# Kernel optimization log

Measured on AMD Instinct MI355X. Metric: run time of the kernel, lower is better.

Reference implementation:

```python
import jax, jax.numpy as jnp
import numpy as np

B, T, E = 4, 2048, 2048
NH, NKV, HD = 16, 4, 128
THETA = 10000.0


def _rope(x, pos_ids, theta):
    # x: [b, h, t, hd]; pos_ids: [b, t]; theta: [hd/2]
    ang = pos_ids[:, None, :, None].astype(jnp.float32) * theta  # [b,1,t,hd/2]
    cos, sin = jnp.cos(ang), jnp.sin(ang)
    x1, x2 = x[..., ::2], x[..., 1::2]
    # interleave rotated pairs back to [..., hd]
    rot = jnp.stack([x1 * cos - x2 * sin, x1 * sin + x2 * cos], axis=-1)
    return rot.reshape(x.shape)


def setup_inputs() -> dict:
    key = jax.random.key(0)
    ks = jax.random.split(key, 10)
    s = 0.02
    x = jax.random.normal(ks[0], (B, T, E), dtype=jnp.float32)
    attention_mask = jax.random.randint(ks[1], (B, T, T), 0, 2, dtype=jnp.int32)
    # torch nn.Linear weights stored here as [in, out] (y = x @ W + b)
    Wq = jax.random.normal(ks[2], (E, E), dtype=jnp.float32) * s
    bq = jnp.zeros((E,), dtype=jnp.float32)
    Wk = jax.random.normal(ks[3], (E, NKV * HD), dtype=jnp.float32) * s
    bk = jnp.zeros((NKV * HD,), dtype=jnp.float32)
    Wv = jax.random.normal(ks[4], (E, NKV * HD), dtype=jnp.float32) * s
    bv = jnp.zeros((NKV * HD,), dtype=jnp.float32)
    Wo = jax.random.normal(ks[5], (E, E), dtype=jnp.float32) * s
    bo = jnp.zeros((E,), dtype=jnp.float32)
    return {"x": x, "attention_mask": attention_mask, "Wq": Wq, "bq": bq,
            "Wk": Wk, "bk": bk, "Wv": Wv, "bv": bv, "Wo": Wo, "bo": bo}


def reference(x, attention_mask, Wq, bq, Wk, bk, Wv, bv, Wo, bo):
    b, t = x.shape[0], x.shape[1]
    # faithful to original: plain reshape (view), NOT transpose-based head split
    q = (x @ Wq + bq).reshape(b, NH, t, HD)
    k = (x @ Wk + bk).reshape(b, NKV, t, HD)
    v = (x @ Wv + bv).reshape(b, NKV, t, HD)
    theta = THETA ** (-jnp.arange(0, HD, 2, dtype=jnp.float32) / HD)
    pos = jnp.broadcast_to(jnp.arange(t), (b, t))
    # original RoPE.forward is wrapped in @torch.no_grad() -> stop_gradient
    k = jax.lax.stop_gradient(_rope(k, pos, theta))
    v = jax.lax.stop_gradient(_rope(v, pos, theta))  # note: RoPE applied to V too
    g = NH // NKV
    k = jnp.tile(k, (1, g, 1, 1))  # torch .repeat tiles kv heads
    v = jnp.tile(v, (1, g, 1, 1))
    # original divides by head_dim ** (-0.5) == multiply by sqrt(head_dim)
    scores = jnp.einsum('bhqd,bhkd->bhqk', q, k) * (HD ** 0.5)
    scores = jnp.where(attention_mask[:, None, :, :] == 0, jnp.float32(1e-9), scores)
    attn = jax.nn.softmax(scores, axis=-1)  # dropout inactive (eval mode)
    out = jnp.einsum('bhqk,bhkd->bhqd', attn, v)
    out = out.transpose(0, 2, 1, 3).reshape(b, t, NH * HD)
    return out @ Wo + bo
```

## Files before the change

kernel.cpp:

```cpp
#include <hip/hip_runtime.h>
#include <math.h>

constexpr int Bc   = 4;
constexpr int Tc   = 2048;
constexpr int Ec   = 2048;
constexpr int NHc  = 16;
constexpr int NKVc = 4;
constexpr int HDc  = 128;
constexpr int KVEc = NKVc * HDc;

typedef __attribute__((ext_vector_type(8))) short bf16x8;
typedef __attribute__((ext_vector_type(4))) short short4v;
typedef __attribute__((ext_vector_type(4))) float f32x4;

__device__ __forceinline__ short f2bf(float f) {
    union { float f; unsigned u; } v; v.f = f;
    unsigned r = v.u + 0x7FFF + ((v.u >> 16) & 1);
    return (short)(r >> 16);
}
__device__ __forceinline__ float bf2f(short s) {
    union { unsigned u; float f; } v; v.u = ((unsigned)(unsigned short)s) << 16;
    return v.f;
}
__device__ __forceinline__ float ex2(float x) {
    float r; asm("v_exp_f32 %0, %1" : "=v"(r) : "v"(x)); return r;
}
__device__ __forceinline__ void gload16(const void* g, void* l) {
    __builtin_amdgcn_global_load_lds(
        (const __attribute__((address_space(1))) unsigned*)g,
        (__attribute__((address_space(3))) unsigned*)l, 16, 0, 0);
}

__global__ __launch_bounds__(256)
void convert_split(const float* __restrict__ X, short* __restrict__ Xhi,
                   short* __restrict__ Xlo)
{
    int i = blockIdx.x * 256 + threadIdx.x;
    float4 v = ((const float4*)X)[i];
    float fv[4] = {v.x, v.y, v.z, v.w};
    short4v hi, lo;
    #pragma unroll
    for (int j = 0; j < 4; ++j) {
        hi[j] = f2bf(fv[j]);
        lo[j] = f2bf(fv[j] - bf2f(hi[j]));
    }
    ((short4v*)Xhi)[i] = hi;
    ((short4v*)Xlo)[i] = lo;
}

__global__ __launch_bounds__(256)
void transpose_split(const float* __restrict__ W, short* __restrict__ WThi,
                     short* __restrict__ WTlo, int K, int N)
{
    __shared__ float Ls[32][33];
    const int k0 = blockIdx.x * 32, n0 = blockIdx.y * 32;
    const int t = threadIdx.x;
    const int r = t >> 3, c4 = (t & 7) << 2;
    float4 v = *(const float4*)(W + (size_t)(k0 + r) * N + n0 + c4);
    Ls[r][c4 + 0] = v.x; Ls[r][c4 + 1] = v.y;
    Ls[r][c4 + 2] = v.z; Ls[r][c4 + 3] = v.w;
    __syncthreads();
    short4v hi, lo;
    #pragma unroll
    for (int i = 0; i < 4; ++i) {
        float f = Ls[c4 + i][r];
        hi[i] = f2bf(f);
        lo[i] = f2bf(f - bf2f(hi[i]));
    }
    *(short4v*)(WThi + (size_t)(n0 + r) * K + k0 + c4) = hi;
    if (WTlo) *(short4v*)(WTlo + (size_t)(n0 + r) * K + k0 + c4) = lo;
}

__global__ __launch_bounds__(256)
void mask_bits(const int* __restrict__ mask, unsigned long long* __restrict__ Mb)
{
    const int widx = blockIdx.x * 4 + (threadIdx.x >> 6);
    const int L = threadIdx.x & 63;
    const int m = mask[(size_t)widx * 64 + L];
    unsigned long long bits = __ballot(m != 0);
    if (L == 0) Mb[widx] = bits;
}

template <bool SPLIT, bool QOUT>
__global__ __launch_bounds__(256, 2)
void gemm_mfma(const short* __restrict__ Ahi, const short* __restrict__ Alo,
               const short* __restrict__ Bhi, const short* __restrict__ Blo,
               const float* __restrict__ bias, float* __restrict__ C,
               short* __restrict__ Chi, short* __restrict__ Clo,
               int M, int N, int K)
{
    __shared__ short AsH[128 * 32];
    __shared__ short BsH[128 * 32];
    __shared__ short AsL[SPLIT ? 128 * 32 : 8];
    __shared__ short BsL[SPLIT ? 128 * 32 : 8];

    const int t = threadIdx.x;
    const int w = t >> 6, L = t & 63;
    const int l16 = L & 15, quad = L >> 4;
    const int wr = w >> 1, wc = w & 1;
    const int bm = blockIdx.x * 128, bn = blockIdx.y * 128;

    const int sm = L >> 2;
    const int sq = ((L & 3) - (sm >> 2)) & 3;
    const int scol = sq * 8;

    f32x4 acc[4][4];
    #pragma unroll
    for (int mi = 0; mi < 4; ++mi)
        #pragma unroll
        for (int ni = 0; ni < 4; ++ni) acc[mi][ni] = (f32x4){0, 0, 0, 0};

    const int fxor = (quad + (l16 >> 2)) & 3;

    for (int k0 = 0; k0 < K; k0 += 32) {
        __syncthreads();
        #pragma unroll
        for (int i = 0; i < 2; ++i) {
            const int wl = w * 2 + i;
            const size_t ra = (size_t)(bm + wl * 16 + sm) * K + k0 + scol;
            const size_t rb = (size_t)(bn + wl * 16 + sm) * K + k0 + scol;
            gload16(Ahi + ra, &AsH[wl * 512]);
            gload16(Bhi + rb, &BsH[wl * 512]);
            if (SPLIT) {
                gload16(Alo + ra, &AsL[wl * 512]);
                gload16(Blo + rb, &BsL[wl * 512]);
            }
        }
        __syncthreads();

        bf16x8 ah[4], bh[4], al[4], bl[4];
        #pragma unroll
        for (int mi = 0; mi < 4; ++mi) {
            const int ch = ((wr * 4 + mi) * 64 + l16 * 4 + fxor) * 8;
            ah[mi] = *(const bf16x8*)&AsH[ch];
            if (SPLIT) al[mi] = *(const bf16x8*)&AsL[ch];
        }
        #pragma unroll
        for (int ni = 0; ni < 4; ++ni) {
            const int ch = ((wc * 4 + ni) * 64 + l16 * 4 + fxor) * 8;
            bh[ni] = *(const bf16x8*)&BsH[ch];
            if (SPLIT) bl[ni] = *(const bf16x8*)&BsL[ch];
        }
        #pragma unroll
        for (int mi = 0; mi < 4; ++mi)
            #pragma unroll
            for (int ni = 0; ni < 4; ++ni) {
                acc[mi][ni] = __builtin_amdgcn_mfma_f32_16x16x32_bf16(
                    ah[mi], bh[ni], acc[mi][ni], 0, 0, 0);
                if (SPLIT) {
                    acc[mi][ni] = __builtin_amdgcn_mfma_f32_16x16x32_bf16(
                        al[mi], bh[ni], acc[mi][ni], 0, 0, 0);
                    acc[mi][ni] = __builtin_amdgcn_mfma_f32_16x16x32_bf16(
                        ah[mi], bl[ni], acc[mi][ni], 0, 0, 0);
                }
            }
    }

    #pragma unroll
    for (int ni = 0; ni < 4; ++ni) {
        const int col = bn + wc * 64 + ni * 16 + l16;
        const float bv = bias[col];
        #pragma unroll
        for (int mi = 0; mi < 4; ++mi) {
            #pragma unroll
            for (int r = 0; r < 4; ++r) {
                const int row = bm + wr * 64 + mi * 16 + quad * 4 + r;
                const float f = acc[mi][ni][r] + bv;
                if (QOUT) {
                    const short hi = f2bf(f);
                    Chi[(size_t)row * N + col] = hi;
                    Clo[(size_t)row * N + col] = f2bf(f - bf2f(hi));
                } else {
                    C[(size_t)row * N + col] = f;
                }
            }
        }
    }
}

__global__ __launch_bounds__(256)
void rope_k(const float* __restrict__ X2d, short* __restrict__ Khi,
            short* __restrict__ Klo)
{
    const int idx = blockIdx.x * 256 + threadIdx.x;
    const int j  = idx & 63;
    const int tk = (idx >> 6) & (Tc - 1);
    const int kh = (idx >> 17) & (NKVc - 1);
    const int bb = idx >> 19;
    const int row = (kh << 9) + (tk >> 2);
    const int col = ((tk & 3) << 7) + (j << 1);
    const float* src = X2d + ((size_t)bb * Tc + row) * KVEc + col;
    const float a = src[0];
    const float b = src[1];
    const float theta = powf(10000.0f, -(float)j * (1.0f / 64.0f));
    const float ang = (float)tk * theta;
    float s, c;
    sincosf(ang, &s, &c);
    const float r0 = a * c - b * s;
    const float r1 = a * s + b * c;
    const size_t off = (((size_t)bb * NKVc + kh) * Tc + tk) * HDc + (j << 1);
    short h0 = f2bf(r0), h1 = f2bf(r1);
    Khi[off]     = h0;  Klo[off]     = f2bf(r0 - bf2f(h0));
    Khi[off + 1] = h1;  Klo[off + 1] = f2bf(r1 - bf2f(h1));
}

__global__ __launch_bounds__(256)
void rope_v_t(const float* __restrict__ V2d, short* __restrict__ Vt)
{
    __shared__ short Ls[128][40];
    const int g  = blockIdx.x;
    const int kh = blockIdx.y;
    const int bb = blockIdx.z;
    const int t  = threadIdx.x;

    const float* src = V2d + ((size_t)bb * Tc + (kh << 9) + (g << 3)) * KVEc;
    #pragma unroll
    for (int i = 0; i < 4; ++i) {
        int e = i * 256 + t;
        float4 v = ((const float4*)src)[e];
        int row = e >> 7;
        int col = (e & 127) << 2;
        int tkl = (row << 2) + (col >> 7);
        int d0  = col & 127;
        int tk  = (g << 5) + tkl;
        float fv[4] = {v.x, v.y, v.z, v.w};
        #pragma unroll
        for (int p = 0; p < 2; ++p) {
            int j = (d0 >> 1) + p;
            float theta = powf(10000.0f, -(float)j * (1.0f / 64.0f));
            float ang = (float)tk * theta;
            float s, c;
            sincosf(ang, &s, &c);
            float a = fv[2 * p], b = fv[2 * p + 1];
            Ls[d0 + 2 * p    ][tkl] = f2bf(a * c - b * s);
            Ls[d0 + 2 * p + 1][tkl] = f2bf(a * s + b * c);
        }
    }
    __syncthreads();
    const int d = t >> 1;
    const int h16 = (t & 1) << 4;
    short* dst = Vt + (((size_t)bb * NKVc + kh) * HDc + d) * Tc + (g << 5) + h16;
    bf16x8 o0 = *(const bf16x8*)&Ls[d][h16];
    bf16x8 o1 = *(const bf16x8*)&Ls[d][h16 + 8];
    *(bf16x8*)dst = o0;
    *(bf16x8*)(dst + 8) = o1;
}

#define SM_AND_P(S, MR, LPV, OACC, MW, AK0, AK1)                               \
  do {                                                                         \
    const unsigned mlo_ = (unsigned)(MW);                                      \
    const unsigned mhi_ = (unsigned)((MW) >> 32);                              \
    const int gq_ = quad << 2;                                                 \
    const unsigned fm_0 = mlo_ >> gq_, fm_1 = (mlo_ >> 16) >> gq_;             \
    const unsigned fm_2 = mhi_ >> gq_, fm_3 = (mhi_ >> 16) >> gq_;             \
    _Pragma("unroll")                                                          \
    for (int r_ = 0; r_ < 4; ++r_) {                                           \
      S[0][r_] = (fm_0 & (1u << r_)) ? S[0][r_] * SCALE2 : MASKED2;            \
      S[1][r_] = (fm_1 & (1u << r_)) ? S[1][r_] * SCALE2 : MASKED2;            \
      S[2][r_] = (fm_2 & (1u << r_)) ? S[2][r_] * SCALE2 : MASKED2;            \
      S[3][r_] = (fm_3 & (1u << r_)) ? S[3][r_] * SCALE2 : MASKED2;            \
    }                                                                          \
    float mt_;                                                                 \
    {                                                                          \
      float a0_ = fmaxf(fmaxf(S[0][0], S[0][1]), fmaxf(S[0][2], S[0][3]));     \
      float a1_ = fmaxf(fmaxf(S[1][0], S[1][1]), fmaxf(S[1][2], S[1][3]));     \
      float a2_ = fmaxf(fmaxf(S[2][0], S[2][1]), fmaxf(S[2][2], S[2][3]));     \
      float a3_ = fmaxf(fmaxf(S[3][0], S[3][1]), fmaxf(S[3][2], S[3][3]));     \
      mt_ = fmaxf(fmaxf(a0_, a1_), fmaxf(a2_, a3_));                           \
    }                                                                          \
    mt_ = fmaxf(mt_, __shfl_xor(mt_, 16));                                     \
    mt_ = fmaxf(mt_, __shfl_xor(mt_, 32));                                     \
    const bool res_ = (mt_ > (MR) + 8.0f);                                     \
    if (__any(res_)) {                                                         \
      const float mn_ = res_ ? mt_ : (MR);                                     \
      const float alq_ = ex2((MR) - mn_);                                      \
      MR = mn_;                                                                \
      LPV *= alq_;                                                             \
      float alo_0 = __shfl(alq_, quad * 20 + 0);                               \
      float alo_1 = __shfl(alq_, quad * 20 + 1);                               \
      float alo_2 = __shfl(alq_, quad * 20 + 2);                               \
      float alo_3 = __shfl(alq_, quad * 20 + 3);                               \
      _Pragma("unroll")                                                        \
      for (int nc_ = 0; nc_ < 8; ++nc_) {                                      \
        OACC[nc_][0] *= alo_0; OACC[nc_][1] *= alo_1;                          \
        OACC[nc_][2] *= alo_2; OACC[nc_][3] *= alo_3;                          \
      }                                                                        \
    }                                                                          \
    {                                                                          \
      float t0_ = 0.f, t1_ = 0.f;                                              \
      _Pragma("unroll")                                                        \
      for (int nt_ = 0; nt_ < 4; ++nt_) {                                      \
        float p0_ = ex2(S[nt_][0] - (MR));                                     \
        float p1_ = ex2(S[nt_][1] - (MR));                                     \
        float p2_ = ex2(S[nt_][2] - (MR));                                     \
        float p3_ = ex2(S[nt_][3] - (MR));                                     \
        S[nt_][0] = p0_; S[nt_][1] = p1_;                                      \
        S[nt_][2] = p2_; S[nt_][3] = p3_;                                      \
        t0_ += p0_ + p1_; t1_ += p2_ + p3_;                                    \
      }                                                                        \
      LPV += t0_ + t1_;                                                        \
    }                                                                          \
    int pk00_, pk01_, pk10_, pk11_, pk20_, pk21_, pk30_, pk31_;                \
    asm("v_cvt_pk_bf16_f32 %0, %1, %2" : "=v"(pk00_) : "v"(S[0][0]), "v"(S[0][1])); \
    asm("v_cvt_pk_bf16_f32 %0, %1, %2" : "=v"(pk01_) : "v"(S[0][2]), "v"(S[0][3])); \
    asm("v_cvt_pk_bf16_f32 %0, %1, %2" : "=v"(pk10_) : "v"(S[1][0]), "v"(S[1][1])); \
    asm("v_cvt_pk_bf16_f32 %0, %1, %2" : "=v"(pk11_) : "v"(S[1][2]), "v"(S[1][3])); \
    asm("v_cvt_pk_bf16_f32 %0, %1, %2" : "=v"(pk20_) : "v"(S[2][0]), "v"(S[2][1])); \
    asm("v_cvt_pk_bf16_f32 %0, %1, %2" : "=v"(pk21_) : "v"(S[2][2]), "v"(S[2][3])); \
    asm("v_cvt_pk_bf16_f32 %0, %1, %2" : "=v"(pk30_) : "v"(S[3][0]), "v"(S[3][1])); \
    asm("v_cvt_pk_bf16_f32 %0, %1, %2" : "=v"(pk31_) : "v"(S[3][2]), "v"(S[3][3])); \
    {                                                                          \
      int u0_, u1_;                                                            \
      u0_ = __shfl(pk00_, srcA); u1_ = __shfl(pk10_, srcA); AK0.d[0] = q1v ? u1_ : u0_; \
      u0_ = __shfl(pk01_, srcA); u1_ = __shfl(pk11_, srcA); AK0.d[1] = q1v ? u1_ : u0_; \
      u0_ = __shfl(pk00_, srcB); u1_ = __shfl(pk10_, srcB); AK0.d[2] = q1v ? u1_ : u0_; \
      u0_ = __shfl(pk01_, srcB); u1_ = __shfl(pk11_, srcB); AK0.d[3] = q1v ? u1_ : u0_; \
      u0_ = __shfl(pk20_, srcA); u1_ = __shfl(pk30_, srcA); AK1.d[0] = q1v ? u1_ : u0_; \
      u0_ = __shfl(pk21_, srcA); u1_ = __shfl(pk31_, srcA); AK1.d[1] = q1v ? u1_ : u0_; \
      u0_ = __shfl(pk20_, srcB); u1_ = __shfl(pk30_, srcB); AK1.d[2] = q1v ? u1_ : u0_; \
      u0_ = __shfl(pk21_, srcB); u1_ = __shfl(pk31_, srcB); AK1.d[3] = q1v ? u1_ : u0_; \
    }                                                                          \
  } while (0)

__global__ __launch_bounds__(256, 2)
void attn_mfma(const short* __restrict__ Qhi_g, const short* __restrict__ Qlo_g,
               const short* __restrict__ Khi_g, const short* __restrict__ Klo_g,
               const short* __restrict__ Vt_g,
               const unsigned long long* __restrict__ Mb, short* __restrict__ AObf)
{
    __shared__ short KhiS[64 * 128];
    __shared__ short KloS[64 * 128];
    __shared__ short VtS [128 * 64];

    const int fid  = blockIdx.x + 16 * (blockIdx.y + 16 * blockIdx.z);
    const int slot = fid >> 3;
    const int grp  = (fid & 7) + 8 * (slot >> 4);
    const int qb   = slot & 15;
    const int h    = grp & 15;
    const int bb   = grp >> 4;

    const int t    = threadIdx.x;
    const int w    = t >> 6;
    const int L    = t & 63;
    const int l16  = L & 15;
    const int quad = L >> 4;
    const int q1v  = quad >> 1;
    const int kh   = h & (NKVc - 1);
    const int tq0  = qb * 128 + w * 16;
    const int tq1  = tq0 + 64;

    bf16x8 qhi0[4], qlo0[4], qhi1[4], qlo1[4];
    {
        const size_t qoff = (size_t)(bb * Tc + h * HDc + qb * 8 + w) * Ec
                          + 128 * l16 + quad * 8;
        const short* qh = Qhi_g + qoff;
        const short* ql = Qlo_g + qoff;
        #pragma unroll
        for (int kc = 0; kc < 4; ++kc) {
            qhi0[kc] = *(const bf16x8*)(qh + kc * 32);
            qlo0[kc] = *(const bf16x8*)(ql + kc * 32);
            qhi1[kc] = *(const bf16x8*)(qh + (size_t)4 * Ec + kc * 32);
            qlo1[kc] = *(const bf16x8*)(ql + (size_t)4 * Ec + kc * 32);
        }
    }

    float m0 = -INFINITY, lp0 = 0.0f;
    float m1 = -INFINITY, lp1 = 0.0f;
    f32x4 o0[8], o1[8];
    #pragma unroll
    for (int nc = 0; nc < 8; ++nc) {
        o0[nc] = (f32x4){0, 0, 0, 0};
        o1[nc] = (f32x4){0, 0, 0, 0};
    }

    const short* kbh = Khi_g + ((size_t)(bb * NKVc + kh)) * Tc * HDc;
    const short* kbl = Klo_g + ((size_t)(bb * NKVc + kh)) * Tc * HDc;
    const short* vb  = Vt_g  + ((size_t)(bb * NKVc + kh)) * HDc * Tc;
    const unsigned long long* mrow0 =
        Mb + ((size_t)(bb * Tc + tq0 + l16)) * (Tc / 64);
    const unsigned long long* mrow1 = mrow0 + (size_t)64 * (Tc / 64);

    constexpr float SCALE2  = 11.313708498984761f * 1.4426950408889634f;
    constexpr float MASKED2 = 1e-9f * 1.4426950408889634f;

    const int km   = L >> 4;
    const int kpos = L & 15;
    const int vm   = L >> 3;
    const int vc   = ((L & 7) - vm) & 7;

    const int srcA = l16 + 16 * ((2 * quad)     & 3);
    const int srcB = l16 + 16 * ((2 * quad + 1) & 3);

    auto stageK = [&](int kt) {
        #pragma unroll
        for (int i = 0; i < 4; ++i) {
            const int wl = w * 4 + i;
            const int krow = wl * 4 + km;
            const int kc_ = (kpos - (krow & 15)) & 15;
            const size_t go = (size_t)(kt * 64 + krow) * HDc + kc_ * 8;
            gload16(kbh + go, &KhiS[wl * 512]);
            gload16(kbl + go, &KloS[wl * 512]);
        }
    };
    auto stageV = [&](int kt) {
        #pragma unroll
        for (int i = 0; i < 4; ++i) {
            const int wl = w * 4 + i;
            const int vrow = wl * 8 + vm;
            gload16(vb + (size_t)vrow * Tc + kt * 64 + vc * 8, &VtS[wl * 512]);
        }
    };

    asm volatile("s_waitcnt vmcnt(0)" ::: "memory");
    __builtin_amdgcn_sched_barrier(0);
    stageK(0);
    __builtin_amdgcn_sched_barrier(0);
    stageV(0);
    __builtin_amdgcn_sched_barrier(0);

    union U { int d[4]; bf16x8 v; };

    for (int kt = 0; kt < Tc / 64; ++kt) {
        const int ktn = (kt + 1) & 31;

        asm volatile("s_waitcnt vmcnt(4)" ::: "memory");
        __builtin_amdgcn_s_barrier();
        __builtin_amdgcn_sched_barrier(0);

        const unsigned long long mw0 = mrow0[kt];
        const unsigned long long mw1 = mrow1[kt];

        f32x4 s0[4], s1[4];
        #pragma unroll
        for (int nt = 0; nt < 4; ++nt) {
            f32x4 a0 = (f32x4){0, 0, 0, 0};
            f32x4 a1 = (f32x4){0, 0, 0, 0};
            #pragma unroll
            for (int kc = 0; kc < 4; ++kc) {
                const int ch = (((nt * 4 + (l16 >> 2)) << 6) + ((l16 & 3) << 4)
                                + ((kc * 4 + quad + l16) & 15)) << 3;
                bf16x8 khiF = *(const bf16x8*)&KhiS[ch];
                bf16x8 kloF = *(const bf16x8*)&KloS[ch];
                a0 = __builtin_amdgcn_mfma_f32_16x16x32_bf16(khiF, qhi0[kc], a0, 0, 0, 0);
                a0 = __builtin_amdgcn_mfma_f32_16x16x32_bf16(khiF, qlo0[kc], a0, 0, 0, 0);
                a0 = __builtin_amdgcn_mfma_f32_16x16x32_bf16(kloF, qhi0[kc], a0, 0, 0, 0);
                a1 = __builtin_amdgcn_mfma_f32_16x16x32_bf16(khiF, qhi1[kc], a1, 0, 0, 0);
                a1 = __builtin_amdgcn_mfma_f32_16x16x32_bf16(khiF, qlo1[kc], a1, 0, 0, 0);
                a1 = __builtin_amdgcn_mfma_f32_16x16x32_bf16(kloF, qhi1[kc], a1, 0, 0, 0);
            }
            s0[nt] = a0;
            s1[nt] = a1;
        }

        asm volatile("s_waitcnt lgkmcnt(0)" ::: "memory");
        __builtin_amdgcn_sched_barrier(0);
        __builtin_amdgcn_s_barrier();
        __builtin_amdgcn_sched_barrier(0);
        stageK(ktn);
        __builtin_amdgcn_sched_barrier(0);

        asm volatile("s_waitcnt vmcnt(8)" ::: "memory");

        U A00, A01, A10, A11;
        SM_AND_P(s0, m0, lp0, o0, mw0, A00, A01);
        SM_AND_P(s1, m1, lp1, o1, mw1, A10, A11);

        __builtin_amdgcn_s_barrier();
        __builtin_amdgcn_sched_barrier(0);

        #pragma unroll
        for (int nc = 0; nc < 8; ++nc) {
            const int rg = (nc * 2 + (l16 >> 3)) << 6;
            const int rm = l16 & 7;
            const int ch0 = (rg + (rm << 3) + ((quad + rm) & 7)) << 3;
            const int ch1 = (rg + (rm << 3) + ((quad + 4 + rm) & 7)) << 3;
            bf16x8 b0 = *(const bf16x8*)&VtS[ch0];
            bf16x8 b1 = *(const bf16x8*)&VtS[ch1];
            o0[nc] = __builtin_amdgcn_mfma_f32_16x16x32_bf16(A00.v, b0, o0[nc], 0, 0, 0);
            o0[nc] = __builtin_amdgcn_mfma_f32_16x16x32_bf16(A01.v, b1, o0[nc], 0, 0, 0);
            o1[nc] = __builtin_amdgcn_mfma_f32_16x16x32_bf16(A10.v, b0, o1[nc], 0, 0, 0);
            o1[nc] = __builtin_amdgcn_mfma_f32_16x16x32_bf16(A11.v, b1, o1[nc], 0, 0, 0);
        }

        asm volatile("s_waitcnt lgkmcnt(0)" ::: "memory");
        __builtin_amdgcn_sched_barrier(0);
        __builtin_amdgcn_s_barrier();
        __builtin_amdgcn_sched_barrier(0);
        stageV(ktn);
        __builtin_amdgcn_sched_barrier(0);
    }

    asm volatile("s_waitcnt vmcnt(0)" ::: "memory");

    lp0 += __shfl_xor(lp0, 16);
    lp0 += __shfl_xor(lp0, 32);
    lp1 += __shfl_xor(lp1, 16);
    lp1 += __shfl_xor(lp1, 32);
    const float invl0 = 1.0f / lp0;
    const float invl1 = 1.0f / lp1;
    float invo0[4], invo1[4];
    #pragma unroll
    for (int r = 0; r < 4; ++r) {
        invo0[r] = __shfl(invl0, quad * 16 + quad * 4 + r);
        invo1[r] = __shfl(invl1, quad * 16 + quad * 4 + r);
    }

    #pragma unroll
    for (int r = 0; r < 4; ++r) {
        short* orow = AObf + ((size_t)(bb * Tc + tq0 + quad * 4 + r)) * Ec
                           + h * HDc + l16;
        #pragma unroll
        for (int nc = 0; nc < 8; ++nc)
            orow[nc * 16] = f2bf(o0[nc][r] * invo0[r]);
    }
    #pragma unroll
    for (int r = 0; r < 4; ++r) {
        short* orow = AObf + ((size_t)(bb * Tc + tq1 + quad * 4 + r)) * Ec
                           + h * HDc + l16;
        #pragma unroll
        for (int nc = 0; nc < 8; ++nc)
            orow[nc * 16] = f2bf(o1[nc][r] * invo1[r]);
    }
}

extern "C" void kernel_launch(void* const* d_in, const int* in_sizes, int n_in,
                              void* d_out, int out_size, void* d_ws, size_t ws_size,
                              hipStream_t stream)
{
    const float* x    = (const float*)d_in[0];
    const int*  amask = (const int*)  d_in[1];
    const float* Wq   = (const float*)d_in[2];
    const float* bq   = (const float*)d_in[3];
    const float* Wk   = (const float*)d_in[4];
    const float* bk   = (const float*)d_in[5];
    const float* Wv   = (const float*)d_in[6];
    const float* bv   = (const float*)d_in[7];
    const float* Wo   = (const float*)d_in[8];
    const float* bo   = (const float*)d_in[9];
    float* out = (float*)d_out;

    char* ws = (char*)d_ws;
    short* Qhi   = (short*)(ws);
    short* Qlo   = (short*)(ws + 33554432);
    short* Xhi   = (short*)(ws + 67108864);
    short* Xlo   = (short*)(ws + 100663296);
    short* WqThi = (short*)(ws + 134217728);
    short* WqTlo = (short*)(ws + 134217728 + 8388608);
    float* K2d   = (float*)(ws + 150994944);
    float* V2d   = (float*)(ws + 100663296);
    short* Khi   = (short*)(ws + 100663296 + 16777216);
    short* Klo   = (short*)(ws + 100663296 + 25165824);
    short* WkThi = (short*)(ws + 134217728);
    short* WkTlo = (short*)(ws + 134217728 + 2097152);
    short* WvThi = (short*)(ws + 134217728 + 4194304);
    short* WoThi = (short*)(ws + 134217728 + 8388608);
    short* Vt    = (short*)(ws + 150994944);
    short* AObf  = (short*)(ws + 67108864);
    unsigned long long* Mb = (unsigned long long*)(ws + 167772160);

    const int M = Bc * Tc;
    dim3 blk(256);

    mask_bits<<<(Bc * Tc * (Tc / 64)) / 4, blk, 0, stream>>>(amask, Mb);
    transpose_split<<<dim3(Ec / 32, Ec / 32), blk, 0, stream>>>(Wq, WqThi, WqTlo, Ec, Ec);
    convert_split<<<(M * Ec / 4) / 256, blk, 0, stream>>>(x, Xhi, Xlo);
    gemm_mfma<true, true><<<dim3(M / 128, Ec / 128), blk, 0, stream>>>(
        Xhi, Xlo, WqThi, WqTlo, bq, nullptr, Qhi, Qlo, M, Ec, Ec);
    transpose_split<<<dim3(Ec / 32, KVEc / 32), blk, 0, stream>>>(Wk, WkThi, WkTlo, Ec, KVEc);
    transpose_split<<<dim3(Ec / 32, KVEc / 32), blk, 0, stream>>>(Wv, WvThi, nullptr, Ec, KVEc);
    transpose_split<<<dim3(Ec / 32, Ec / 32), blk, 0, stream>>>(Wo, WoThi, nullptr, Ec, Ec);
    gemm_mfma<true, false><<<dim3(M / 128, KVEc / 128), blk, 0, stream>>>(
        Xhi, Xlo, WkThi, WkTlo, bk, K2d, nullptr, nullptr, M, KVEc, Ec);
    gemm_mfma<false, false><<<dim3(M / 128, KVEc / 128), blk, 0, stream>>>(
        Xhi, nullptr, WvThi, nullptr, bv, V2d, nullptr, nullptr, M, KVEc, Ec);
    rope_k<<<(Bc * NKVc * Tc * 64) / 256, blk, 0, stream>>>(K2d, Khi, Klo);
    rope_v_t<<<dim3(Tc / 32, NKVc, Bc), blk, 0, stream>>>(V2d, Vt);
    attn_mfma<<<dim3(Tc / 128, NHc, Bc), blk, 0, stream>>>(
        Qhi, Qlo, Khi, Klo, Vt, Mb, AObf);
    gemm_mfma<false, false><<<dim3(M / 128, Ec / 128), blk, 0, stream>>>(
        AObf, nullptr, WoThi, nullptr, bo, out, nullptr, nullptr, M, Ec, Ec);
}
```

Measured before the change: 1.049 ms.

## Software-pipeline PV product one tile behind softmax with double-buffered V

Splits the softmax macro into mask/max, rescale and exp/convert parts, then issues the P·V MFMAs for the previous key tile while the current tile's exponentials are computed. V shared memory is double-buffered so the previous tile's V stays resident, and a final PV flush runs after the loop. The aim is to overlap MFMA work with the softmax VALU work and drop one barrier per iteration. The cost is doubled V LDS, extra registers for the carried P fragments, and a branchy path where a rescale forces the previous PV before the correction is applied.

```diff
diff --git a/kernel.cpp b/kernel.cpp
--- a/kernel.cpp
+++ b/kernel.cpp
@@ -246,7 +246,7 @@
     *(bf16x8*)(dst + 8) = o1;
 }
 
-#define SM_AND_P(S, MR, LPV, OACC, MW, AK0, AK1)                               \
+#define MASK_MAX(S, MW, MT)                                                    \
   do {                                                                         \
     const unsigned mlo_ = (unsigned)(MW);                                      \
     const unsigned mhi_ = (unsigned)((MW) >> 32);                              \
@@ -260,32 +260,36 @@
       S[2][r_] = (fm_2 & (1u << r_)) ? S[2][r_] * SCALE2 : MASKED2;            \
       S[3][r_] = (fm_3 & (1u << r_)) ? S[3][r_] * SCALE2 : MASKED2;            \
     }                                                                          \
-    float mt_;                                                                 \
     {                                                                          \
       float a0_ = fmaxf(fmaxf(S[0][0], S[0][1]), fmaxf(S[0][2], S[0][3]));     \
       float a1_ = fmaxf(fmaxf(S[1][0], S[1][1]), fmaxf(S[1][2], S[1][3]));     \
       float a2_ = fmaxf(fmaxf(S[2][0], S[2][1]), fmaxf(S[2][2], S[2][3]));     \
       float a3_ = fmaxf(fmaxf(S[3][0], S[3][1]), fmaxf(S[3][2], S[3][3]));     \
-      mt_ = fmaxf(fmaxf(a0_, a1_), fmaxf(a2_, a3_));                           \
+      MT = fmaxf(fmaxf(a0_, a1_), fmaxf(a2_, a3_));                            \
     }                                                                          \
-    mt_ = fmaxf(mt_, __shfl_xor(mt_, 16));                                     \
-    mt_ = fmaxf(mt_, __shfl_xor(mt_, 32));                                     \
-    const bool res_ = (mt_ > (MR) + 8.0f);                                     \
-    if (__any(res_)) {                                                         \
-      const float mn_ = res_ ? mt_ : (MR);                                     \
-      const float alq_ = ex2((MR) - mn_);                                      \
-      MR = mn_;                                                                \
-      LPV *= alq_;                                                             \
-      float alo_0 = __shfl(alq_, quad * 20 + 0);                               \
-      float alo_1 = __shfl(alq_, quad * 20 + 1);                               \
-      float alo_2 = __shfl(alq_, quad * 20 + 2);                               \
-      float alo_3 = __shfl(alq_, quad * 20 + 3);                               \
-      _Pragma("unroll")                                                        \
-      for (int nc_ = 0; nc_ < 8; ++nc_) {                                      \
-        OACC[nc_][0] *= alo_0; OACC[nc_][1] *= alo_1;                          \
-        OACC[nc_][2] *= alo_2; OACC[nc_][3] *= alo_3;                          \
-      }                                                                        \
+    MT = fmaxf(MT, __shfl_xor(MT, 16));                                        \
+    MT = fmaxf(MT, __shfl_xor(MT, 32));                                        \
+  } while (0)
+
+#define RESCALE1(MR, MT, RES, LPV, OACC)                                       \
+  do {                                                                         \
+    const float mn_ = (RES) ? (MT) : (MR);                                     \
+    const float alq_ = ex2((MR) - mn_);                                        \
+    MR = mn_;                                                                  \
+    LPV *= alq_;                                                               \
+    float alo_0 = __shfl(alq_, quad * 20 + 0);                                 \
+    float alo_1 = __shfl(alq_, quad * 20 + 1);                                 \
+    float alo_2 = __shfl(alq_, quad * 20 + 2);                                 \
+    float alo_3 = __shfl(alq_, quad * 20 + 3);                                 \
+    _Pragma("unroll")                                                          \
+    for (int nc_ = 0; nc_ < 8; ++nc_) {                                        \
+      OACC[nc_][0] *= alo_0; OACC[nc_][1] *= alo_1;                            \
+      OACC[nc_][2] *= alo_2; OACC[nc_][3] *= alo_3;                            \
     }                                                                          \
+  } while (0)
+
+#define EXP_CVT(S, MR, LPV, AK0, AK1)                                          \
+  do {                                                                         \
     {                                                                          \
       float t0_ = 0.f, t1_ = 0.f;                                              \
       _Pragma("unroll")                                                        \
@@ -322,6 +326,23 @@
     }                                                                          \
   } while (0)
 
+#define PV_PREV(VB)                                                            \
+  do {                                                                         \
+    _Pragma("unroll")                                                          \
+    for (int nc_ = 0; nc_ < 8; ++nc_) {                                        \
+      const int rg_ = (nc_ * 2 + (l16 >> 3)) << 6;                             \
+      const int rm_ = l16 & 7;                                                 \
+      const int c0_ = (rg_ + (rm_ << 3) + ((quad + rm_) & 7)) << 3;            \
+      const int c1_ = (rg_ + (rm_ << 3) + ((quad + 4 + rm_) & 7)) << 3;        \
+      bf16x8 b0_ = *(const bf16x8*)&(VB)[c0_];                                 \
+      bf16x8 b1_ = *(const bf16x8*)&(VB)[c1_];                                 \
+      o0[nc_] = __builtin_amdgcn_mfma_f32_16x16x32_bf16(Ap00.v, b0_, o0[nc_], 0, 0, 0); \
+      o0[nc_] = __builtin_amdgcn_mfma_f32_16x16x32_bf16(Ap01.v, b1_, o0[nc_], 0, 0, 0); \
+      o1[nc_] = __builtin_amdgcn_mfma_f32_16x16x32_bf16(Ap10.v, b0_, o1[nc_], 0, 0, 0); \
+      o1[nc_] = __builtin_amdgcn_mfma_f32_16x16x32_bf16(Ap11.v, b1_, o1[nc_], 0, 0, 0); \
+    }                                                                          \
+  } while (0)
+
 __global__ __launch_bounds__(256, 2)
 void attn_mfma(const short* __restrict__ Qhi_g, const short* __restrict__ Qlo_g,
                const short* __restrict__ Khi_g, const short* __restrict__ Klo_g,
@@ -330,7 +351,7 @@
 {
     __shared__ short KhiS[64 * 128];
     __shared__ short KloS[64 * 128];
-    __shared__ short VtS [128 * 64];
+    __shared__ short VtS [2][128 * 64];
 
     const int fid  = blockIdx.x + 16 * (blockIdx.y + 16 * blockIdx.z);
     const int slot = fid >> 3;
@@ -402,26 +423,35 @@
             gload16(kbl + go, &KloS[wl * 512]);
         }
     };
-    auto stageV = [&](int kt) {
+    auto stageV = [&](int kt, int buf) {
         #pragma unroll
         for (int i = 0; i < 4; ++i) {
             const int wl = w * 4 + i;
             const int vrow = wl * 8 + vm;
-            gload16(vb + (size_t)vrow * Tc + kt * 64 + vc * 8, &VtS[wl * 512]);
+            gload16(vb + (size_t)vrow * Tc + kt * 64 + vc * 8,
+                    &VtS[buf][wl * 512]);
         }
     };
+
+    union U { int d[4]; bf16x8 v; };
+    U Ap00, Ap01, Ap10, Ap11;
+    #pragma unroll
+    for (int i = 0; i < 4; ++i) {
+        Ap00.d[i] = 0; Ap01.d[i] = 0; Ap10.d[i] = 0; Ap11.d[i] = 0;
+    }
 
     asm volatile("s_waitcnt vmcnt(0)" ::: "memory");
     __builtin_amdgcn_sched_barrier(0);
     stageK(0);
     __builtin_amdgcn_sched_barrier(0);
-    stageV(0);
+    stageV(0, 0);
+    stageV(0, 1);
     __builtin_amdgcn_sched_barrier(0);
-
-    union U { int d[4]; bf16x8 v; };
 
     for (int kt = 0; kt < Tc / 64; ++kt) {
         const int ktn = (kt + 1) & 31;
+        const int pb  = (kt + 1) & 1;
+        const short* vbp = &VtS[pb][0];
 
         asm volatile("s_waitcnt vmcnt(4)" ::: "memory");
         __builtin_amdgcn_s_barrier();
@@ -461,36 +491,40 @@
 
         asm volatile("s_waitcnt vmcnt(8)" ::: "memory");
 
-        U A00, A01, A10, A11;
-        SM_AND_P(s0, m0, lp0, o0, mw0, A00, A01);
-        SM_AND_P(s1, m1, lp1, o1, mw1, A10, A11);
-
-        __builtin_amdgcn_s_barrier();
-        __builtin_amdgcn_sched_barrier(0);
-
-        #pragma unroll
-        for (int nc = 0; nc < 8; ++nc) {
-            const int rg = (nc * 2 + (l16 >> 3)) << 6;
-            const int rm = l16 & 7;
-            const int ch0 = (rg + (rm << 3) + ((quad + rm) & 7)) << 3;
-            const int ch1 = (rg + (rm << 3) + ((quad + 4 + rm) & 7)) << 3;
-            bf16x8 b0 = *(const bf16x8*)&VtS[ch0];
-            bf16x8 b1 = *(const bf16x8*)&VtS[ch1];
-            o0[nc] = __builtin_amdgcn_mfma_f32_16x16x32_bf16(A00.v, b0, o0[nc], 0, 0, 0);
-            o0[nc] = __builtin_amdgcn_mfma_f32_16x16x32_bf16(A01.v, b1, o0[nc], 0, 0, 0);
-            o1[nc] = __builtin_amdgcn_mfma_f32_16x16x32_bf16(A10.v, b0, o1[nc], 0, 0, 0);
-            o1[nc] = __builtin_amdgcn_mfma_f32_16x16x32_bf16(A11.v, b1, o1[nc], 0, 0, 0);
-        }
+        float mt0, mt1;
+        MASK_MAX(s0, mw0, mt0);
+        MASK_MAX(s1, mw1, mt1);
+        const bool res0 = (mt0 > m0 + 8.0f);
+        const bool res1 = (mt1 > m1 + 8.0f);
+        bool flushed = false;
+        if (__any(res0 || res1)) {
+            PV_PREV(vbp);
+            RESCALE1(m0, mt0, res0, lp0, o0);
+            RESCALE1(m1, mt1, res1, lp1, o1);
+            flushed = true;
+        }
+
+        U An00, An01, An10, An11;
+        EXP_CVT(s0, m0, lp0, An00, An01);
+        EXP_CVT(s1, m1, lp1, An10, An11);
+
+        if (!flushed) PV_PREV(vbp);
 
         asm volatile("s_waitcnt lgkmcnt(0)" ::: "memory");
         __builtin_amdgcn_sched_barrier(0);
         __builtin_amdgcn_s_barrier();
         __builtin_amdgcn_sched_barrier(0);
-        stageV(ktn);
+        stageV(ktn, pb);
         __builtin_amdgcn_sched_barrier(0);
+
+        Ap00 = An00; Ap01 = An01; Ap10 = An10; Ap11 = An11;
     }
 
     asm volatile("s_waitcnt vmcnt(0)" ::: "memory");
+    {
+        const short* vbp = &VtS[1][0];
+        PV_PREV(vbp);
+    }
 
     lp0 += __shfl_xor(lp0, 16);
     lp0 += __shfl_xor(lp0, 32);
```

Result: slower. 1.115 ms (+6.3%).
